# Performance work log

Measured on AMD Instinct MI355X. Metric: run time of the kernel, lower is better.

Reference implementation:

```python
import jax, jax.numpy as jnp
import numpy as np

NUM_ATOMS = 40000
NUM_EDGES = 640000
FAN_IN = 128
NFM = 128
FAN_OUT = 128


def setup_inputs() -> dict:
    key = jax.random.key(0)
    k1, k2, k3, k4, k5, k6, k7 = jax.random.split(key, 7)
    x = jax.random.normal(k1, (NUM_ATOMS, FAN_IN), dtype=jnp.float32)
    w_ij = jax.random.normal(k2, (NUM_EDGES, NFM), dtype=jnp.float32)
    seg_i = jnp.sort(jax.random.randint(k3, (NUM_EDGES,), 0, NUM_ATOMS))
    idx_j = jax.random.randint(k4, (NUM_EDGES,), 0, NUM_ATOMS)
    # learned params: in2fac (no bias), fac2out (bias)
    W_in = jax.random.normal(k5, (FAN_IN, NFM), dtype=jnp.float32) / np.sqrt(FAN_IN)
    W_out = jax.random.normal(k6, (NFM, FAN_OUT), dtype=jnp.float32) / np.sqrt(NFM)
    b_out = jax.random.normal(k7, (FAN_OUT,), dtype=jnp.float32) * 0.01
    return {"x": x, "w_ij": w_ij, "seg_i": seg_i, "idx_j": idx_j,
            "seg_i_sum": NUM_ATOMS, "W_in": W_in, "W_out": W_out, "b_out": b_out}


def reference(x, w_ij, seg_i, idx_j, seg_i_sum, W_in, W_out, b_out):
    # in2fac: Dense without bias  (num_atoms, nFM)
    f = x @ W_in
    # gather features of atom j per interaction  (num_edges, nFM)
    f_j = jnp.take(f, idx_j, axis=0)
    # elementwise filter multiply
    wf = w_ij * f_j
    # segment-sum pool over interactions of each atom i  (num_atoms, nFM)
    conv = jax.ops.segment_sum(wf, seg_i, num_segments=seg_i_sum)
    # fac2out: Dense with bias, activation=None
    return conv @ W_out + b_out
```

## Files before the change

### kernel.cpp

```cpp
#include <hip/hip_runtime.h>

#define NUM_ATOMS 40000
#define NUM_EDGES 640000

__global__ void k_rowstart(const int* __restrict__ seg, int* __restrict__ rs) {
  const int i = blockIdx.x * blockDim.x + threadIdx.x;
  if (i > NUM_ATOMS) return;
  int lo = 0, hi = NUM_EDGES;
  while (lo < hi) {
    const int mid = (lo + hi) >> 1;
    if (seg[mid] < i) lo = mid + 1; else hi = mid;
  }
  rs[i] = lo;
}

__global__ __launch_bounds__(512, 2) void k_gemm128(
    const float* __restrict__ A, const float* __restrict__ W,
    const float* __restrict__ bias, float* __restrict__ out) {
  __shared__ float AT[128 * 128];
  __shared__ float Wl[128 * 128];
  const int t = threadIdx.x;
  const int m0 = blockIdx.x * 128;

  {
    const float4* Wg = (const float4*)W;
    float4* Ws = (float4*)Wl;
#pragma unroll
    for (int i = 0; i < 8; ++i) Ws[t + i * 512] = Wg[t + i * 512];
  }
  {
    const int m = t & 127;
    const int kq = t >> 7;
    int mg = m0 + m;
    if (mg >= NUM_ATOMS) mg = NUM_ATOMS - 1;
    const float4* ag = (const float4*)(A + (size_t)mg * 128);
#pragma unroll
    for (int i = 0; i < 8; ++i) {
      const int k4 = kq + i * 4;
      const float4 v = ag[k4];
      const int k = k4 * 4;
      AT[(k + 0) * 128 + m] = v.x;
      AT[(k + 1) * 128 + m] = v.y;
      AT[(k + 2) * 128 + m] = v.z;
      AT[(k + 3) * 128 + m] = v.w;
    }
  }
  __syncthreads();

  const int tx = t & 31;
  const int ty = t >> 5;

  float binit[4] = {0.f, 0.f, 0.f, 0.f};
  if (bias != nullptr) {
    const float2 bb0 = ((const float2*)bias)[tx];
    const float2 bb1 = ((const float2*)bias)[32 + tx];
    binit[0] = bb0.x; binit[1] = bb0.y; binit[2] = bb1.x; binit[3] = bb1.y;
  }
  float acc[8][4];
#pragma unroll
  for (int i = 0; i < 8; ++i)
#pragma unroll
    for (int j = 0; j < 4; ++j) acc[i][j] = binit[j];

#pragma unroll 4
  for (int k = 0; k < 128; ++k) {
    const float4 a0 = *(const float4*)&AT[k * 128 + 4 * ty];
    const float4 a1 = *(const float4*)&AT[k * 128 + 64 + 4 * ty];
    const float2 b0 = *(const float2*)&Wl[k * 128 + 2 * tx];
    const float2 b1 = *(const float2*)&Wl[k * 128 + 64 + 2 * tx];
    const float av[8] = {a0.x, a0.y, a0.z, a0.w, a1.x, a1.y, a1.z, a1.w};
    const float bv[4] = {b0.x, b0.y, b1.x, b1.y};
#pragma unroll
    for (int i = 0; i < 8; ++i)
#pragma unroll
      for (int j = 0; j < 4; ++j) acc[i][j] += av[i] * bv[j];
  }

#pragma unroll
  for (int i = 0; i < 8; ++i) {
    const int m = (i < 4) ? (4 * ty + i) : (64 + 4 * ty + (i - 4));
    const int mg = m0 + m;
    if (mg < NUM_ATOMS) {
      float2* o = (float2*)(out + (size_t)mg * 128);
      o[tx]      = make_float2(acc[i][0], acc[i][1]);
      o[32 + tx] = make_float2(acc[i][2], acc[i][3]);
    }
  }
}

__global__ __launch_bounds__(256) void k_conv(
    const float* __restrict__ f, const float* __restrict__ w_ij,
    const int* __restrict__ idx_j, const int* __restrict__ rs,
    float* __restrict__ conv) {
  const int wv = threadIdx.x >> 6;
  const int l = threadIdx.x & 63;
  const int a = blockIdx.x * 4 + wv;

  const int e0 = rs[a];
  const int e1 = rs[a + 1];
  float accx = 0.f, accy = 0.f;

  for (int base = e0; base < e1; base += 32) {
    const int n = min(32, e1 - base);
    const int nm1 = n - 1;
    int j = 0;
    if (l < n) j = idx_j[base + l];

    float2 wr[32], fr[32];
#pragma unroll
    for (int g = 0; g < 4; ++g) {
      if (n > g * 8) {
#pragma unroll
        for (int k = g * 8; k < g * 8 + 8; ++k) {
          const int kk = min(k, nm1);
          wr[k] = ((const float2*)(w_ij + (size_t)(base + kk) * 128))[l];
        }
      }
    }
#pragma unroll
    for (int g = 0; g < 4; ++g) {
      if (n > g * 8) {
#pragma unroll
        for (int k = g * 8; k < g * 8 + 8; ++k) {
          const int kk = min(k, nm1);
          const int jk = __shfl(j, kk);
          fr[k] = ((const float2*)(f + (size_t)jk * 128))[l];
        }
      }
    }
#pragma unroll
    for (int g = 0; g < 4; ++g) {
      if (n > g * 8) {
#pragma unroll
        for (int k = g * 8; k < g * 8 + 8; ++k) {
          if (k < n) {
            accx += wr[k].x * fr[k].x;
            accy += wr[k].y * fr[k].y;
          }
        }
      }
    }
  }
  ((float2*)(conv + (size_t)a * 128))[l] = make_float2(accx, accy);
}

extern "C" void kernel_launch(void* const* d_in, const int* in_sizes, int n_in,
                              void* d_out, int out_size, void* d_ws, size_t ws_size,
                              hipStream_t stream) {
  const float* x    = (const float*)d_in[0];
  const float* w_ij = (const float*)d_in[1];
  const int*   seg  = (const int*)d_in[2];
  const int*   idxj = (const int*)d_in[3];
  const float* Win  = (const float*)d_in[5];
  const float* Wout = (const float*)d_in[6];
  const float* bout = (const float*)d_in[7];
  float* out = (float*)d_out;

  float* f    = (float*)d_ws;
  float* conv = (float*)((char*)d_ws + (size_t)NUM_ATOMS * 128 * sizeof(float));
  int*   rs   = (int*)((char*)d_ws + 2 * (size_t)NUM_ATOMS * 128 * sizeof(float));

  k_rowstart<<<(NUM_ATOMS + 1 + 255) / 256, 256, 0, stream>>>(seg, rs);
  k_gemm128<<<(NUM_ATOMS + 127) / 128, 512, 0, stream>>>(x, Win, nullptr, f);
  k_conv<<<NUM_ATOMS / 4, 256, 0, stream>>>(f, w_ij, idxj, rs, conv);
  k_gemm128<<<(NUM_ATOMS + 127) / 128, 512, 0, stream>>>(conv, Wout, bout, out);
}
```

Measured before the change: 545.2 us.

## Fuse row-start search into first GEMM launch and halve GEMM shared memory

The binary-search row-start computation is merged into the first GEMM launch as extra blocks, which removes one kernel launch. The GEMM now loads K in two 64-wide halves, so shared memory per block drops from 128 KB to 64 KB and the launch bound is raised to 4 blocks per CU for higher occupancy. In exchange each block gains an extra sync and reload phase, and W is staged twice per block.

```diff
diff --git a/kernel.cpp b/kernel.cpp
--- a/kernel.cpp
+++ b/kernel.cpp
@@ -3,49 +3,19 @@
 #define NUM_ATOMS 40000
 #define NUM_EDGES 640000
 
-__global__ void k_rowstart(const int* __restrict__ seg, int* __restrict__ rs) {
-  const int i = blockIdx.x * blockDim.x + threadIdx.x;
-  if (i > NUM_ATOMS) return;
-  int lo = 0, hi = NUM_EDGES;
-  while (lo < hi) {
-    const int mid = (lo + hi) >> 1;
-    if (seg[mid] < i) lo = mid + 1; else hi = mid;
-  }
-  rs[i] = lo;
-}
+#define GEMM_BLOCKS 313
+#define RS_BLOCKS 79
 
-__global__ __launch_bounds__(512, 2) void k_gemm128(
+__device__ __forceinline__ void gemm128_body(
     const float* __restrict__ A, const float* __restrict__ W,
-    const float* __restrict__ bias, float* __restrict__ out) {
-  __shared__ float AT[128 * 128];
-  __shared__ float Wl[128 * 128];
-  const int t = threadIdx.x;
-  const int m0 = blockIdx.x * 128;
-
-  {
-    const float4* Wg = (const float4*)W;
-    float4* Ws = (float4*)Wl;
-#pragma unroll
-    for (int i = 0; i < 8; ++i) Ws[t + i * 512] = Wg[t + i * 512];
-  }
-  {
-    const int m = t & 127;
-    const int kq = t >> 7;
-    int mg = m0 + m;
-    if (mg >= NUM_ATOMS) mg = NUM_ATOMS - 1;
-    const float4* ag = (const float4*)(A + (size_t)mg * 128);
-#pragma unroll
-    for (int i = 0; i < 8; ++i) {
-      const int k4 = kq + i * 4;
-      const float4 v = ag[k4];
-      const int k = k4 * 4;
-      AT[(k + 0) * 128 + m] = v.x;
-      AT[(k + 1) * 128 + m] = v.y;
-      AT[(k + 2) * 128 + m] = v.z;
-      AT[(k + 3) * 128 + m] = v.w;
-    }
-  }
-  __syncthreads();
+    const float* __restrict__ bias, float* __restrict__ out,
+    float* AT, float* Wl, int bid, int t) {
+  const int m0 = bid * 128;
+  const int m = t & 127;
+  const int kq = t >> 7;
+  int mg = m0 + m;
+  if (mg >= NUM_ATOMS) mg = NUM_ATOMS - 1;
+  const float4* ag = (const float4*)(A + (size_t)mg * 128);
 
   const int tx = t & 31;
   const int ty = t >> 5;
@@ -62,30 +32,83 @@
 #pragma unroll
     for (int j = 0; j < 4; ++j) acc[i][j] = binit[j];
 
+#pragma unroll
+  for (int kh = 0; kh < 2; ++kh) {
+    const int k0 = kh * 64;
+    {
+      const float4* Wg = (const float4*)(W + (size_t)k0 * 128);
+      float4* Ws4 = (float4*)Wl;
+#pragma unroll
+      for (int i = 0; i < 4; ++i) Ws4[t + i * 512] = Wg[t + i * 512];
+    }
+#pragma unroll
+    for (int i = 0; i < 4; ++i) {
+      const int c = kq + 4 * i;
+      const float4 v = ag[(k0 >> 2) + c];
+      const int k = 4 * c;
+      AT[(k + 0) * 128 + m] = v.x;
+      AT[(k + 1) * 128 + m] = v.y;
+      AT[(k + 2) * 128 + m] = v.z;
+      AT[(k + 3) * 128 + m] = v.w;
+    }
+    __syncthreads();
+
 #pragma unroll 4
-  for (int k = 0; k < 128; ++k) {
-    const float4 a0 = *(const float4*)&AT[k * 128 + 4 * ty];
-    const float4 a1 = *(const float4*)&AT[k * 128 + 64 + 4 * ty];
-    const float2 b0 = *(const float2*)&Wl[k * 128 + 2 * tx];
-    const float2 b1 = *(const float2*)&Wl[k * 128 + 64 + 2 * tx];
-    const float av[8] = {a0.x, a0.y, a0.z, a0.w, a1.x, a1.y, a1.z, a1.w};
-    const float bv[4] = {b0.x, b0.y, b1.x, b1.y};
+    for (int k = 0; k < 64; ++k) {
+      const float4 a0 = *(const float4*)&AT[k * 128 + 4 * ty];
+      const float4 a1 = *(const float4*)&AT[k * 128 + 64 + 4 * ty];
+      const float2 b0 = *(const float2*)&Wl[k * 128 + 2 * tx];
+      const float2 b1 = *(const float2*)&Wl[k * 128 + 64 + 2 * tx];
+      const float av[8] = {a0.x, a0.y, a0.z, a0.w, a1.x, a1.y, a1.z, a1.w};
+      const float bv[4] = {b0.x, b0.y, b1.x, b1.y};
 #pragma unroll
-    for (int i = 0; i < 8; ++i)
+      for (int i = 0; i < 8; ++i)
 #pragma unroll
-      for (int j = 0; j < 4; ++j) acc[i][j] += av[i] * bv[j];
+        for (int j = 0; j < 4; ++j) acc[i][j] += av[i] * bv[j];
+    }
+    __syncthreads();
   }
 
 #pragma unroll
   for (int i = 0; i < 8; ++i) {
-    const int m = (i < 4) ? (4 * ty + i) : (64 + 4 * ty + (i - 4));
-    const int mg = m0 + m;
-    if (mg < NUM_ATOMS) {
-      float2* o = (float2*)(out + (size_t)mg * 128);
+    const int mm = (i < 4) ? (4 * ty + i) : (64 + 4 * ty + (i - 4));
+    const int mg2 = m0 + mm;
+    if (mg2 < NUM_ATOMS) {
+      float2* o = (float2*)(out + (size_t)mg2 * 128);
       o[tx]      = make_float2(acc[i][0], acc[i][1]);
       o[32 + tx] = make_float2(acc[i][2], acc[i][3]);
     }
   }
+}
+
+__global__ __launch_bounds__(512, 4) void k_pre(
+    const float* __restrict__ A, const float* __restrict__ W,
+    float* __restrict__ out,
+    const int* __restrict__ seg, int* __restrict__ rs) {
+  __shared__ float AT[64 * 128];
+  __shared__ float Wl[64 * 128];
+  const int t = threadIdx.x;
+  if (blockIdx.x >= GEMM_BLOCKS) {
+    const int i = (blockIdx.x - GEMM_BLOCKS) * 512 + t;
+    if (i <= NUM_ATOMS) {
+      int lo = 0, hi = NUM_EDGES;
+      while (lo < hi) {
+        const int mid = (lo + hi) >> 1;
+        if (seg[mid] < i) lo = mid + 1; else hi = mid;
+      }
+      rs[i] = lo;
+    }
+    return;
+  }
+  gemm128_body(A, W, nullptr, out, AT, Wl, blockIdx.x, t);
+}
+
+__global__ __launch_bounds__(512, 4) void k_out(
+    const float* __restrict__ A, const float* __restrict__ W,
+    const float* __restrict__ bias, float* __restrict__ out) {
+  __shared__ float AT[64 * 128];
+  __shared__ float Wl[64 * 128];
+  gemm128_body(A, W, bias, out, AT, Wl, blockIdx.x, threadIdx.x);
 }
 
 __global__ __launch_bounds__(256) void k_conv(
@@ -160,8 +183,7 @@
   float* conv = (float*)((char*)d_ws + (size_t)NUM_ATOMS * 128 * sizeof(float));
   int*   rs   = (int*)((char*)d_ws + 2 * (size_t)NUM_ATOMS * 128 * sizeof(float));
 
-  k_rowstart<<<(NUM_ATOMS + 1 + 255) / 256, 256, 0, stream>>>(seg, rs);
-  k_gemm128<<<(NUM_ATOMS + 127) / 128, 512, 0, stream>>>(x, Win, nullptr, f);
+  k_pre<<<GEMM_BLOCKS + RS_BLOCKS, 512, 0, stream>>>(x, Win, f, seg, rs);
   k_conv<<<NUM_ATOMS / 4, 256, 0, stream>>>(f, w_ij, idxj, rs, conv);
-  k_gemm128<<<(NUM_ATOMS + 127) / 128, 512, 0, stream>>>(conv, Wout, bout, out);
+  k_out<<<GEMM_BLOCKS, 512, 0, stream>>>(conv, Wout, bout, out);
 }
```

Result: faster. 518.5 us (-4.9%).
